# Kernel optimization log

Hardware: AMD Instinct MI355X
Metric: run time of the kernel (lower is better)

## Reference

```python
import jax, jax.numpy as jnp
import numpy as np

B, M_IN, H, W = 8, 63, 480, 640
VALID_FRAC = 0.05  # sparse-depth valid pixel density
N_ITERS = 5


def setup_inputs() -> dict:
    key = jax.random.key(0)
    k1, k2, k3 = jax.random.split(key, 3)
    bases = jax.random.normal(k1, (B, M_IN, H, W), dtype=jnp.float32)
    logit = jax.random.normal(k2, (B, 1, H, W), dtype=jnp.float32)
    valid = jax.random.uniform(k3, (B, 1, H, W)) < VALID_FRAC
    # invalid sparse-depth pixels -> log(0) = -inf, ignored via isfinite mask
    targets = jnp.where(valid, logit, -jnp.inf)
    return {"bases": bases, "targets": targets}


def _fit_single(basis, target):
    # basis: (m,h,w), target: (1,h,w)
    m = basis.shape[0]
    y = target[0]                                   # (h,w)
    mask = jnp.isfinite(y)
    maskf = mask.astype(basis.dtype)
    Xf = (basis * maskf).reshape(m, -1)             # masked basis, (m, hw)
    yf = jnp.where(mask, y, 0.0).reshape(-1)        # (hw,)
    XtX = Xf @ Xf.T                                 # (m,m) over valid pixels only
    Xty = Xf @ yf                                   # (m,)
    N = maskf.sum()

    # eval-mode EM-like refinement (prior.use == False): Tr_d = M / beta
    beta0 = jnp.sqrt(N)
    beta = beta0
    done = jnp.array(False)
    for _ in range(N_ITERS):
        w = jnp.linalg.solve(XtX * beta, Xty * beta)    # LU solve
        E_d = jnp.sum((yf - w @ Xf) ** 2)               # residual on valid pixels
        Tr_d = m / beta
        beta_new = N / (E_d + Tr_d)
        conv = jnp.abs(beta_new / beta0 - 1.0) < 0.02
        beta = jnp.where(done, beta, beta_new)
        beta0 = jnp.where(done, beta0, beta_new)
        done = done | conv

    A = XtX * beta
    w = jnp.linalg.solve(A, Xty * beta)                 # (m,)

    # recon3d: predicted log depth
    logit_pred = jnp.einsum('m,mhw->hw', w, basis)[None]  # (1,h,w)

    # pred_var: S_inv via Cholesky, var = (S_inv @ bt * bt).sum(0)
    L = jnp.linalg.cholesky(A)
    S_inv = jax.scipy.linalg.cho_solve((L, True), jnp.eye(m, dtype=basis.dtype))
    bt = basis.reshape(m, -1)                           # (m, hw)
    var = jnp.sum((S_inv @ bt) * bt, axis=0).reshape(1, basis.shape[1], basis.shape[2])
    return logit_pred, w, var


def reference(bases, targets):
    # th_homogenize(append=False): prepend a constant ones basis channel
    ones = jnp.ones_like(bases[:, :1])
    basis_h = jnp.concatenate([ones, bases], axis=1)    # (b, m+1, h, w)
    logits, weights, logit_var = jax.vmap(_fit_single)(basis_h, targets)
    return logits, weights, logit_var
```

## Files before the change

kernel.cpp:

```cpp
#include <hip/hip_runtime.h>
#include <cmath>

#define HW 307200
#define NB 8
#define NBASE 63
#define NCHUNK (HW/256)
#define GRAM_BLKS 128
#define QCAP 320

#define XTY_OFF 0
#define YTY_OFF (NB*64)
#define NC_OFF  (YTY_OFF + NB)
#define ZERO_FLOATS (NC_OFF + NB)
#define XTX_OFF ZERO_FLOATS
#define MP_OFF  (XTX_OFF + NB*64*64)
#define WV_OFF  (MP_OFF + NB*64*64)

#define OUT_W   (NB*HW)
#define OUT_VAR (OUT_W + NB*64)

__device__ __forceinline__ bool finitef(float x) {
    return (__float_as_uint(x) & 0x7f800000u) != 0x7f800000u;
}

__global__ __launch_bounds__(256) void gram_kernel(
    const float* __restrict__ bases, const float* __restrict__ targets,
    float* __restrict__ ws, float* __restrict__ part)
{
    __shared__ float tile[64*68];
    __shared__ float sy[64];
    __shared__ float qy[QCAP];
    __shared__ int   qidx[QCAP];
    __shared__ int   qn;

    const int t  = threadIdx.x;
    const int b  = blockIdx.y;
    const int wv = t >> 6;
    const int l  = t & 63;
    const int ti = l >> 3, tj = l & 7;

    float acc[8][8];
#pragma unroll
    for (int i = 0; i < 8; i++)
#pragma unroll
        for (int j = 0; j < 8; j++) acc[i][j] = 0.f;
    float acc_xty = 0.f, acc_yty = 0.f, acc_n = 0.f;

    const float* __restrict__ basesb = bases + (long)b * NBASE * HW;
    const float* __restrict__ targb  = targets + (long)b * HW;
    const long choff = (long)(l - 1) * HW;

    if (t == 0) qn = 0;
    __syncthreads();

    auto compute_tile = [&]() {
#pragma unroll 2
        for (int pp = 0; pp < 16; ++pp) {
            const int p2 = wv * 16 + pp;
            const float4 r0 = *(const float4*)&tile[p2*68 + 8*ti];
            const float4 r1 = *(const float4*)&tile[p2*68 + 8*ti + 4];
            const float4 c0 = *(const float4*)&tile[p2*68 + 8*tj];
            const float4 c1 = *(const float4*)&tile[p2*68 + 8*tj + 4];
            const float rr[8] = {r0.x,r0.y,r0.z,r0.w,r1.x,r1.y,r1.z,r1.w};
            const float cc[8] = {c0.x,c0.y,c0.z,c0.w,c1.x,c1.y,c1.z,c1.w};
#pragma unroll
            for (int i = 0; i < 8; i++)
#pragma unroll
                for (int j = 0; j < 8; j++)
                    acc[i][j] = fmaf(rr[i], cc[j], acc[i][j]);
            acc_xty = fmaf(sy[p2], tile[p2*68 + l], acc_xty);
        }
    };

    int qtot = 0;
    for (int j = blockIdx.x; j < NCHUNK; j += GRAM_BLKS) {
        const int p = j * 256 + t;
        const float y = targb[p];
        const bool fin = finitef(y);
        const unsigned long long m = __ballot(fin);
        int wbase = 0;
        if (l == 0) wbase = atomicAdd(&qn, __popcll(m));
        wbase = __shfl(wbase, 0, 64);
        if (fin) {
            const int r = __popcll(m & ((1ull << l) - 1ull));
            qidx[wbase + r] = p;
            qy[wbase + r]   = y;
            acc_yty = fmaf(y, y, acc_yty);
            acc_n += 1.f;
        }
        __syncthreads();
        qtot = qn;
        while (qtot >= 64) {
            const int base = qtot - 64;
            if (t < 64) sy[t] = qy[base + t];
#pragma unroll
            for (int pp = wv; pp < 64; pp += 4) {
                const int gp = qidx[base + pp];
                float v;
                if (l == 0) v = 1.f;
                else        v = basesb[choff + gp];
                tile[pp*68 + l] = v;
            }
            __syncthreads();
            compute_tile();
            qtot -= 64;
            __syncthreads();
        }
        if (t == 0) qn = qtot;
        __syncthreads();
    }

    if (qtot > 0) {
        if (t < 64) sy[t] = (t < qtot) ? qy[t] : 0.f;
#pragma unroll
        for (int pp = wv; pp < 64; pp += 4) {
            float v = 0.f;
            if (pp < qtot) {
                const int gp = qidx[pp];
                if (l == 0) v = 1.f;
                else        v = basesb[choff + gp];
            }
            tile[pp*68 + l] = v;
        }
        __syncthreads();
        compute_tile();
    }
    __syncthreads();

    for (int w = 0; w < 4; ++w) {
        if (wv == w) {
#pragma unroll
            for (int i = 0; i < 8; i++)
#pragma unroll
                for (int j2 = 0; j2 < 8; j2++) {
                    const int e = (8*ti + i) * 64 + 8*tj + j2;
                    tile[e] = (w == 0) ? acc[i][j2] : tile[e] + acc[i][j2];
                }
        }
        __syncthreads();
    }
    float* __restrict__ pb = part + (long)(b * GRAM_BLKS + blockIdx.x) * 4096;
#pragma unroll
    for (int k = 0; k < 4; ++k)
        *(float4*)&pb[t*16 + 4*k] = *(const float4*)&tile[t*16 + 4*k];

    for (int w = 0; w < 4; ++w) {
        if (wv == w) tile[4096 + l] = (w == 0) ? acc_xty : tile[4096 + l] + acc_xty;
        __syncthreads();
    }
    if (t < 64) atomicAdd(&ws[XTY_OFF + b*64 + t], tile[4096 + t]);

#pragma unroll
    for (int off = 32; off; off >>= 1) {
        acc_yty += __shfl_down(acc_yty, off, 64);
        acc_n   += __shfl_down(acc_n,   off, 64);
    }
    if (l == 0) {
        atomicAdd(&ws[YTY_OFF + b], acc_yty);
        atomicAdd(&ws[NC_OFF  + b], acc_n);
    }
}

__global__ __launch_bounds__(256) void reduce_kernel(
    const float* __restrict__ part, float* __restrict__ ws)
{
    const int b = blockIdx.y;
    const int e = blockIdx.x * 256 + threadIdx.x;
    const float* __restrict__ pb = part + (long)b * GRAM_BLKS * 4096 + e;
    float s = 0.f;
#pragma unroll 8
    for (int k = 0; k < GRAM_BLKS; ++k)
        s += pb[(long)k * 4096];
    ws[XTX_OFF + b*4096 + e] = s;
}

__global__ __launch_bounds__(64) void solve_kernel(
    float* __restrict__ ws, float* __restrict__ out)
{
    __shared__ float A[64*65];
    __shared__ float W[64*65];
    __shared__ float d0[64], xty[64], wv_s[64];

    const int b = blockIdx.x;
    const int t = threadIdx.x;
    const float* XtX = ws + XTX_OFF + b * 4096;

    for (int j = 0; j < 64; j++) A[t*65 + j] = XtX[t*64 + j];
    xty[t] = ws[XTY_OFF + b*64 + t];
    d0[t]  = A[t*65 + t];
    const float yty = ws[YTY_OFF + b];
    const float Nc  = ws[NC_OFF  + b];
    __syncthreads();

    for (int k = 0; k < 64; k++) {
        float akk = A[k*65 + k];
        __syncthreads();
        float dk = sqrtf(akk);
        if (t == k)      A[k*65 + k] = dk;
        else if (t > k)  A[t*65 + k] = A[t*65 + k] / dk;
        __syncthreads();
        if (t > k) {
            float ltk = A[t*65 + k];
            for (int j = k + 1; j <= t; j++)
                A[t*65 + j] -= ltk * A[j*65 + k];
        }
        __syncthreads();
    }

    for (int i = 0; i < 64; i++) {
        float s = (i == t) ? 1.f : 0.f;
        for (int j = 0; j < i; j++) s = fmaf(-A[i*65 + j], W[j*65 + t], s);
        W[i*65 + t] = s / A[i*65 + i];
    }
    for (int i = 63; i >= 0; i--) {
        float s = W[i*65 + t];
        for (int j = i + 1; j < 64; j++) s = fmaf(-A[j*65 + i], W[j*65 + t], s);
        W[i*65 + t] = s / A[i*65 + i];
    }
    __syncthreads();

    float wt = 0.f;
    for (int j = 0; j < 64; j++) wt = fmaf(W[t*65 + j], xty[j], wt);
    wv_s[t] = wt;
    __syncthreads();

    float qt = 0.f;
    for (int j = 0; j < 64; j++) {
        float x = (j > t) ? A[t*65 + j] : ((j == t) ? d0[t] : A[j*65 + t]);
        qt = fmaf(x, wv_s[j], qt);
    }
    float r1 = wt * xty[t];
    float r2 = wt * qt;
#pragma unroll
    for (int off = 32; off; off >>= 1) {
        r1 += __shfl_down(r1, off, 64);
        r2 += __shfl_down(r2, off, 64);
    }
    r1 = __shfl(r1, 0, 64);
    r2 = __shfl(r2, 0, 64);
    const float E_d = yty - 2.f * r1 + r2;

    float beta0 = sqrtf(Nc);
    float beta  = beta0;
    bool  done  = false;
#pragma unroll
    for (int it = 0; it < 5; ++it) {
        float Tr_d = 64.f / beta;
        float beta_new = Nc / (E_d + Tr_d);
        bool conv = fabsf(beta_new / beta0 - 1.f) < 0.02f;
        if (!done) { beta = beta_new; beta0 = beta_new; }
        done = done || conv;
    }
    const float ib = 1.f / beta;

    out[OUT_W + b*64 + t] = wt;
    ws[WV_OFF + b*64 + t] = wt;
    float* Mp = ws + MP_OFF + b * 4096;
    for (int j = 0; j < 64; j++) {
        float v = (j < t) ? 0.f : ((j == t) ? 0.5f : 1.f) * W[t*65 + j] * ib;
        Mp[t*64 + j] = v;
    }
}

__global__ __launch_bounds__(256) void predvar_kernel(
    const float* __restrict__ bases, const float* __restrict__ ws,
    float* __restrict__ out)
{
    const int b   = blockIdx.y;
    const int pix = blockIdx.x * 256 + threadIdx.x;
    const float* __restrict__ Mp = ws + MP_OFF + b * 4096;
    const float* __restrict__ wb = ws + WV_OFF + b * 64;
    const float* basesb = bases + (long)b * NBASE * HW + pix;

    float bv[64];
    bv[0] = 1.f;
#pragma unroll
    for (int c = 1; c < 64; c++) bv[c] = basesb[(long)(c - 1) * HW];

    float pred = wb[0];
#pragma unroll
    for (int c = 1; c < 64; c++) pred = fmaf(wb[c], bv[c], pred);

    float var2 = 0.f;
#pragma unroll
    for (int i = 0; i < 64; i++) {
        float si = 0.f;
#pragma unroll
        for (int j = i; j < 64; j++) si = fmaf(Mp[i*64 + j], bv[j], si);
        var2 = fmaf(si, bv[i], var2);
    }

    out[(long)b * HW + pix] = pred;
    out[OUT_VAR + (long)b * HW + pix] = 2.f * var2;
}

extern "C" void kernel_launch(void* const* d_in, const int* in_sizes, int n_in,
                              void* d_out, int out_size, void* d_ws, size_t ws_size,
                              hipStream_t stream)
{
    const float* bases   = (const float*)d_in[0];
    const float* targets = (const float*)d_in[1];
    float* out = (float*)d_out;
    float* ws  = (float*)d_ws;

    hipMemsetAsync(d_ws, 0, ZERO_FLOATS * sizeof(float), stream);

    gram_kernel<<<dim3(GRAM_BLKS, NB), 256, 0, stream>>>(bases, targets, ws, out);
    reduce_kernel<<<dim3(16, NB), 256, 0, stream>>>(out, ws);
    solve_kernel<<<NB, 64, 0, stream>>>(ws, out);
    predvar_kernel<<<dim3(HW / 256, NB), 256, 0, stream>>>(bases, ws, out);
}
```

Before: 579.1 us.

## Stage Mp in LDS, process two pixels per thread, widen Cholesky block

The pred-var kernel now copies the per-batch packed inverse matrix into shared memory and reads it as float4. Each thread handles two adjacent pixels with float2 loads, so every matrix element fetched is reused for two pixels. The solve kernel moves from 64 to 256 threads and splits the Cholesky trailing update and the final Mp write-out across four thread groups. The cost is a larger register footprint (two 64-float vectors per thread) under launch_bounds(256,2), which may cause spills or lower occupancy.

```diff
diff --git a/kernel.cpp b/kernel.cpp
--- a/kernel.cpp
+++ b/kernel.cpp
@@ -174,124 +174,158 @@
     ws[XTX_OFF + b*4096 + e] = s;
 }
 
-__global__ __launch_bounds__(64) void solve_kernel(
+__global__ __launch_bounds__(256) void solve_kernel(
     float* __restrict__ ws, float* __restrict__ out)
 {
     __shared__ float A[64*65];
     __shared__ float W[64*65];
-    __shared__ float d0[64], xty[64], wv_s[64];
+    __shared__ float d0[64], xty_s[64], wv_s[64];
+    __shared__ float ib_s;
 
     const int b = blockIdx.x;
     const int t = threadIdx.x;
+    const int r = t & 63;
+    const int q = t >> 6;
     const float* XtX = ws + XTX_OFF + b * 4096;
 
-    for (int j = 0; j < 64; j++) A[t*65 + j] = XtX[t*64 + j];
-    xty[t] = ws[XTY_OFF + b*64 + t];
-    d0[t]  = A[t*65 + t];
+    for (int e = t; e < 4096; e += 256)
+        A[(e >> 6) * 65 + (e & 63)] = XtX[e];
+    if (t < 64) xty_s[t] = ws[XTY_OFF + b*64 + t];
     const float yty = ws[YTY_OFF + b];
     const float Nc  = ws[NC_OFF  + b];
     __syncthreads();
+    if (t < 64) d0[t] = A[t*65 + t];
+    __syncthreads();
 
     for (int k = 0; k < 64; k++) {
-        float akk = A[k*65 + k];
-        __syncthreads();
-        float dk = sqrtf(akk);
-        if (t == k)      A[k*65 + k] = dk;
-        else if (t > k)  A[t*65 + k] = A[t*65 + k] / dk;
-        __syncthreads();
-        if (t > k) {
-            float ltk = A[t*65 + k];
-            for (int j = k + 1; j <= t; j++)
-                A[t*65 + j] -= ltk * A[j*65 + k];
-        }
-        __syncthreads();
-    }
-
-    for (int i = 0; i < 64; i++) {
-        float s = (i == t) ? 1.f : 0.f;
-        for (int j = 0; j < i; j++) s = fmaf(-A[i*65 + j], W[j*65 + t], s);
-        W[i*65 + t] = s / A[i*65 + i];
-    }
-    for (int i = 63; i >= 0; i--) {
-        float s = W[i*65 + t];
-        for (int j = i + 1; j < 64; j++) s = fmaf(-A[j*65 + i], W[j*65 + t], s);
-        W[i*65 + t] = s / A[i*65 + i];
-    }
-    __syncthreads();
-
-    float wt = 0.f;
-    for (int j = 0; j < 64; j++) wt = fmaf(W[t*65 + j], xty[j], wt);
-    wv_s[t] = wt;
-    __syncthreads();
-
-    float qt = 0.f;
-    for (int j = 0; j < 64; j++) {
-        float x = (j > t) ? A[t*65 + j] : ((j == t) ? d0[t] : A[j*65 + t]);
-        qt = fmaf(x, wv_s[j], qt);
-    }
-    float r1 = wt * xty[t];
-    float r2 = wt * qt;
-#pragma unroll
-    for (int off = 32; off; off >>= 1) {
-        r1 += __shfl_down(r1, off, 64);
-        r2 += __shfl_down(r2, off, 64);
-    }
-    r1 = __shfl(r1, 0, 64);
-    r2 = __shfl(r2, 0, 64);
-    const float E_d = yty - 2.f * r1 + r2;
-
-    float beta0 = sqrtf(Nc);
-    float beta  = beta0;
-    bool  done  = false;
-#pragma unroll
-    for (int it = 0; it < 5; ++it) {
-        float Tr_d = 64.f / beta;
-        float beta_new = Nc / (E_d + Tr_d);
-        bool conv = fabsf(beta_new / beta0 - 1.f) < 0.02f;
-        if (!done) { beta = beta_new; beta0 = beta_new; }
-        done = done || conv;
-    }
-    const float ib = 1.f / beta;
-
-    out[OUT_W + b*64 + t] = wt;
-    ws[WV_OFF + b*64 + t] = wt;
-    float* Mp = ws + MP_OFF + b * 4096;
-    for (int j = 0; j < 64; j++) {
-        float v = (j < t) ? 0.f : ((j == t) ? 0.5f : 1.f) * W[t*65 + j] * ib;
-        Mp[t*64 + j] = v;
-    }
-}
-
-__global__ __launch_bounds__(256) void predvar_kernel(
+        const float akk = A[k*65 + k];
+        __syncthreads();
+        const float dk = sqrtf(akk);
+        if (q == 0) {
+            if (r == k)     A[k*65 + k] = dk;
+            else if (r > k) A[r*65 + k] /= dk;
+        }
+        __syncthreads();
+        if (r > k) {
+            const float lrk = A[r*65 + k];
+            for (int j = k + 1 + q; j <= r; j += 4)
+                A[r*65 + j] -= lrk * A[j*65 + k];
+        }
+        __syncthreads();
+    }
+
+    if (q == 0) {
+        for (int i = 0; i < 64; i++) {
+            float s = (i == r) ? 1.f : 0.f;
+            for (int j = 0; j < i; j++) s = fmaf(-A[i*65 + j], W[j*65 + r], s);
+            W[i*65 + r] = s / A[i*65 + i];
+        }
+        for (int i = 63; i >= 0; i--) {
+            float s = W[i*65 + r];
+            for (int j = i + 1; j < 64; j++) s = fmaf(-A[j*65 + i], W[j*65 + r], s);
+            W[i*65 + r] = s / A[i*65 + i];
+        }
+        float wt = 0.f;
+        for (int j = 0; j < 64; j++) wt = fmaf(W[r*65 + j], xty_s[j], wt);
+        wv_s[r] = wt;
+
+        float qt = 0.f;
+        for (int j = 0; j < 64; j++) {
+            float x = (j > r) ? A[r*65 + j] : ((j == r) ? d0[r] : A[j*65 + r]);
+            qt = fmaf(x, wv_s[j], qt);
+        }
+        float r1 = wt * xty_s[r];
+        float r2 = wt * qt;
+#pragma unroll
+        for (int off = 32; off; off >>= 1) {
+            r1 += __shfl_down(r1, off, 64);
+            r2 += __shfl_down(r2, off, 64);
+        }
+        if (r == 0) {
+            const float E_d = yty - 2.f * r1 + r2;
+            float beta0 = sqrtf(Nc);
+            float beta  = beta0;
+            bool  done  = false;
+#pragma unroll
+            for (int it = 0; it < 5; ++it) {
+                float Tr_d = 64.f / beta;
+                float beta_new = Nc / (E_d + Tr_d);
+                bool conv = fabsf(beta_new / beta0 - 1.f) < 0.02f;
+                if (!done) { beta = beta_new; beta0 = beta_new; }
+                done = done || conv;
+            }
+            ib_s = 1.f / beta;
+        }
+        out[OUT_W + b*64 + r] = wt;
+        ws[WV_OFF + b*64 + r] = wt;
+    }
+    __syncthreads();
+
+    const float ib = ib_s;
+    float* __restrict__ Mp = ws + MP_OFF + b * 4096;
+    for (int e = t; e < 4096; e += 256) {
+        const int row = e >> 6, j = e & 63;
+        const float v = (j < row) ? 0.f
+                      : ((j == row) ? 0.5f : 1.f) * W[row*65 + j] * ib;
+        Mp[e] = v;
+    }
+}
+
+__global__ __launch_bounds__(256, 2) void predvar_kernel(
     const float* __restrict__ bases, const float* __restrict__ ws,
     float* __restrict__ out)
 {
-    const int b   = blockIdx.y;
-    const int pix = blockIdx.x * 256 + threadIdx.x;
-    const float* __restrict__ Mp = ws + MP_OFF + b * 4096;
-    const float* __restrict__ wb = ws + WV_OFF + b * 64;
+    __shared__ float Mp_s[4096];
+    __shared__ float w_s[64];
+
+    const int b = blockIdx.y;
+    const int t = threadIdx.x;
+    {
+        const float4* __restrict__ src = (const float4*)(ws + MP_OFF + b * 4096);
+        float4* dst = (float4*)Mp_s;
+        for (int e = t; e < 1024; e += 256) dst[e] = src[e];
+        if (t < 64) w_s[t] = ws[WV_OFF + b*64 + t];
+    }
+    __syncthreads();
+
+    const int pix = (blockIdx.x * 256 + t) * 2;
     const float* basesb = bases + (long)b * NBASE * HW + pix;
 
-    float bv[64];
-    bv[0] = 1.f;
-#pragma unroll
-    for (int c = 1; c < 64; c++) bv[c] = basesb[(long)(c - 1) * HW];
-
-    float pred = wb[0];
-#pragma unroll
-    for (int c = 1; c < 64; c++) pred = fmaf(wb[c], bv[c], pred);
-
-    float var2 = 0.f;
+    float2 bv[64];
+    bv[0] = make_float2(1.f, 1.f);
+#pragma unroll
+    for (int c = 1; c < 64; c++)
+        bv[c] = *(const float2*)&basesb[(long)(c - 1) * HW];
+
+    float px = w_s[0], py = w_s[0];
+#pragma unroll
+    for (int c = 1; c < 64; c++) {
+        px = fmaf(w_s[c], bv[c].x, px);
+        py = fmaf(w_s[c], bv[c].y, py);
+    }
+
+    float vx = 0.f, vy = 0.f;
 #pragma unroll
     for (int i = 0; i < 64; i++) {
-        float si = 0.f;
-#pragma unroll
-        for (int j = i; j < 64; j++) si = fmaf(Mp[i*64 + j], bv[j], si);
-        var2 = fmaf(si, bv[i], var2);
-    }
-
-    out[(long)b * HW + pix] = pred;
-    out[OUT_VAR + (long)b * HW + pix] = 2.f * var2;
+        float sx = 0.f, sy2 = 0.f;
+#pragma unroll
+        for (int qd = i >> 2; qd < 16; qd++) {
+            const float4 m = *(const float4*)&Mp_s[i*64 + 4*qd];
+            sx  = fmaf(m.x, bv[4*qd+0].x, sx);
+            sy2 = fmaf(m.x, bv[4*qd+0].y, sy2);
+            sx  = fmaf(m.y, bv[4*qd+1].x, sx);
+            sy2 = fmaf(m.y, bv[4*qd+1].y, sy2);
+            sx  = fmaf(m.z, bv[4*qd+2].x, sx);
+            sy2 = fmaf(m.z, bv[4*qd+2].y, sy2);
+            sx  = fmaf(m.w, bv[4*qd+3].x, sx);
+            sy2 = fmaf(m.w, bv[4*qd+3].y, sy2);
+        }
+        vx = fmaf(sx,  bv[i].x, vx);
+        vy = fmaf(sy2, bv[i].y, vy);
+    }
+
+    *(float2*)&out[(long)b * HW + pix] = make_float2(px, py);
+    *(float2*)&out[OUT_VAR + (long)b * HW + pix] = make_float2(2.f * vx, 2.f * vy);
 }
 
 extern "C" void kernel_launch(void* const* d_in, const int* in_sizes, int n_in,
@@ -307,6 +341,6 @@
 
     gram_kernel<<<dim3(GRAM_BLKS, NB), 256, 0, stream>>>(bases, targets, ws, out);
     reduce_kernel<<<dim3(16, NB), 256, 0, stream>>>(out, ws);
-    solve_kernel<<<NB, 64, 0, stream>>>(ws, out);
-    predvar_kernel<<<dim3(HW / 256, NB), 256, 0, stream>>>(bases, ws, out);
-}
+    solve_kernel<<<NB, 256, 0, stream>>>(ws, out);
+    predvar_kernel<<<dim3(HW / 512, NB), 256, 0, stream>>>(bases, ws, out);
+}
```

After: 578.3 us. Within noise of the previous version (-0.1%).

## Register-block predvar over 4 pixels with LDS-staged matrix; register-based triangular inverse

Applied to the files above, without the earlier changes.

The pred/var kernel now processes four pixels per thread with float4 loads and stores, and stages the per-batch quadratic-form matrix in shared memory so each matrix element is reused across four pixels. The solve kernel keeps each thread's inverse column in registers, with unrolled multi-accumulator loops and reciprocal diagonals, and writes the matrix transposed for coalesced stores. The aim is to cut instruction and memory overhead in the dominant per-pixel quadratic form. The risk is very high register pressure from 64 float4 values per thread, which may spill or reduce occupancy.

```diff
diff --git a/kernel.cpp b/kernel.cpp
--- a/kernel.cpp
+++ b/kernel.cpp
@@ -178,58 +178,95 @@
     float* __restrict__ ws, float* __restrict__ out)
 {
     __shared__ float A[64*65];
-    __shared__ float W[64*65];
-    __shared__ float d0[64], xty[64], wv_s[64];
+    __shared__ float d0[64], dinv_s[64], xty_s[64], wv_s[64];
 
     const int b = blockIdx.x;
     const int t = threadIdx.x;
     const float* XtX = ws + XTX_OFF + b * 4096;
 
-    for (int j = 0; j < 64; j++) A[t*65 + j] = XtX[t*64 + j];
-    xty[t] = ws[XTY_OFF + b*64 + t];
-    d0[t]  = A[t*65 + t];
+    for (int e = t; e < 4096; e += 64)
+        A[(e >> 6) * 65 + (e & 63)] = XtX[e];
+    xty_s[t] = ws[XTY_OFF + b*64 + t];
     const float yty = ws[YTY_OFF + b];
     const float Nc  = ws[NC_OFF  + b];
     __syncthreads();
+    d0[t] = A[t*65 + t];
+    __syncthreads();
 
     for (int k = 0; k < 64; k++) {
-        float akk = A[k*65 + k];
-        __syncthreads();
-        float dk = sqrtf(akk);
+        const float akk = A[k*65 + k];
+        __syncthreads();
+        const float dk = sqrtf(akk);
         if (t == k)      A[k*65 + k] = dk;
-        else if (t > k)  A[t*65 + k] = A[t*65 + k] / dk;
+        else if (t > k)  A[t*65 + k] /= dk;
         __syncthreads();
         if (t > k) {
-            float ltk = A[t*65 + k];
+            const float ltk = A[t*65 + k];
             for (int j = k + 1; j <= t; j++)
                 A[t*65 + j] -= ltk * A[j*65 + k];
         }
         __syncthreads();
     }
 
+    dinv_s[t] = 1.f / A[t*65 + t];
+    __syncthreads();
+
+    float Wc[64];
+#pragma unroll
     for (int i = 0; i < 64; i++) {
-        float s = (i == t) ? 1.f : 0.f;
-        for (int j = 0; j < i; j++) s = fmaf(-A[i*65 + j], W[j*65 + t], s);
-        W[i*65 + t] = s / A[i*65 + i];
-    }
+        float s0 = (i == t) ? 1.f : 0.f, s1 = 0.f, s2 = 0.f, s3 = 0.f;
+        const int nfull = i >> 2;
+#pragma unroll
+        for (int qd = 0; qd < nfull; qd++) {
+            const int j = qd * 4;
+            s0 = fmaf(-A[i*65 + j    ], Wc[j    ], s0);
+            s1 = fmaf(-A[i*65 + j + 1], Wc[j + 1], s1);
+            s2 = fmaf(-A[i*65 + j + 2], Wc[j + 2], s2);
+            s3 = fmaf(-A[i*65 + j + 3], Wc[j + 3], s3);
+        }
+#pragma unroll
+        for (int j = nfull * 4; j < i; j++)
+            s0 = fmaf(-A[i*65 + j], Wc[j], s0);
+        Wc[i] = ((s0 + s1) + (s2 + s3)) * dinv_s[i];
+    }
+#pragma unroll
     for (int i = 63; i >= 0; i--) {
-        float s = W[i*65 + t];
-        for (int j = i + 1; j < 64; j++) s = fmaf(-A[j*65 + i], W[j*65 + t], s);
-        W[i*65 + t] = s / A[i*65 + i];
-    }
-    __syncthreads();
-
-    float wt = 0.f;
-    for (int j = 0; j < 64; j++) wt = fmaf(W[t*65 + j], xty[j], wt);
+        float s0 = Wc[i], s1 = 0.f, s2 = 0.f, s3 = 0.f;
+        const int j0 = i + 1;
+        const int nfull = (64 - j0) >> 2;
+#pragma unroll
+        for (int qd = 0; qd < nfull; qd++) {
+            const int j = j0 + qd * 4;
+            s0 = fmaf(-A[(j    )*65 + i], Wc[j    ], s0);
+            s1 = fmaf(-A[(j + 1)*65 + i], Wc[j + 1], s1);
+            s2 = fmaf(-A[(j + 2)*65 + i], Wc[j + 2], s2);
+            s3 = fmaf(-A[(j + 3)*65 + i], Wc[j + 3], s3);
+        }
+#pragma unroll
+        for (int j = j0 + nfull * 4; j < 64; j++)
+            s0 = fmaf(-A[j*65 + i], Wc[j], s0);
+        Wc[i] = ((s0 + s1) + (s2 + s3)) * dinv_s[i];
+    }
+
+    float w0 = 0.f, w1 = 0.f, w2 = 0.f, w3 = 0.f;
+#pragma unroll
+    for (int j = 0; j < 64; j += 4) {
+        w0 = fmaf(Wc[j    ], xty_s[j    ], w0);
+        w1 = fmaf(Wc[j + 1], xty_s[j + 1], w1);
+        w2 = fmaf(Wc[j + 2], xty_s[j + 2], w2);
+        w3 = fmaf(Wc[j + 3], xty_s[j + 3], w3);
+    }
+    const float wt = (w0 + w1) + (w2 + w3);
     wv_s[t] = wt;
     __syncthreads();
 
     float qt = 0.f;
+#pragma unroll
     for (int j = 0; j < 64; j++) {
-        float x = (j > t) ? A[t*65 + j] : ((j == t) ? d0[t] : A[j*65 + t]);
+        const float x = (j > t) ? A[t*65 + j] : ((j == t) ? d0[t] : A[j*65 + t]);
         qt = fmaf(x, wv_s[j], qt);
     }
-    float r1 = wt * xty[t];
+    float r1 = wt * xty_s[t];
     float r2 = wt * qt;
 #pragma unroll
     for (int off = 32; off; off >>= 1) {
@@ -245,9 +282,9 @@
     bool  done  = false;
 #pragma unroll
     for (int it = 0; it < 5; ++it) {
-        float Tr_d = 64.f / beta;
-        float beta_new = Nc / (E_d + Tr_d);
-        bool conv = fabsf(beta_new / beta0 - 1.f) < 0.02f;
+        const float Tr_d = 64.f / beta;
+        const float beta_new = Nc / (E_d + Tr_d);
+        const bool conv = fabsf(beta_new / beta0 - 1.f) < 0.02f;
         if (!done) { beta = beta_new; beta0 = beta_new; }
         done = done || conv;
     }
@@ -255,10 +292,11 @@
 
     out[OUT_W + b*64 + t] = wt;
     ws[WV_OFF + b*64 + t] = wt;
-    float* Mp = ws + MP_OFF + b * 4096;
+    float* __restrict__ Mp = ws + MP_OFF + b * 4096;
+#pragma unroll
     for (int j = 0; j < 64; j++) {
-        float v = (j < t) ? 0.f : ((j == t) ? 0.5f : 1.f) * W[t*65 + j] * ib;
-        Mp[t*64 + j] = v;
+        const float v = (j > t) ? 0.f : ((j == t) ? 0.5f : 1.f) * Wc[j] * ib;
+        Mp[j*64 + t] = v;
     }
 }
 
@@ -266,32 +304,70 @@
     const float* __restrict__ bases, const float* __restrict__ ws,
     float* __restrict__ out)
 {
-    const int b   = blockIdx.y;
-    const int pix = blockIdx.x * 256 + threadIdx.x;
-    const float* __restrict__ Mp = ws + MP_OFF + b * 4096;
-    const float* __restrict__ wb = ws + WV_OFF + b * 64;
+    __shared__ float Mp_s[4096];
+    __shared__ float w_s[64];
+
+    const int b = blockIdx.y;
+    const int t = threadIdx.x;
+    {
+        const float4* __restrict__ src = (const float4*)(ws + MP_OFF + b * 4096);
+        float4* dst = (float4*)Mp_s;
+        for (int e = t; e < 1024; e += 256) dst[e] = src[e];
+        if (t < 64) w_s[t] = ws[WV_OFF + b*64 + t];
+    }
+    __syncthreads();
+
+    const int pix = (blockIdx.x * 256 + t) * 4;
     const float* basesb = bases + (long)b * NBASE * HW + pix;
 
-    float bv[64];
-    bv[0] = 1.f;
-#pragma unroll
-    for (int c = 1; c < 64; c++) bv[c] = basesb[(long)(c - 1) * HW];
-
-    float pred = wb[0];
-#pragma unroll
-    for (int c = 1; c < 64; c++) pred = fmaf(wb[c], bv[c], pred);
-
-    float var2 = 0.f;
+    float4 bv[64];
+    bv[0] = make_float4(1.f, 1.f, 1.f, 1.f);
+#pragma unroll
+    for (int c = 1; c < 64; c++)
+        bv[c] = *(const float4*)&basesb[(long)(c - 1) * HW];
+
+    float4 pr = make_float4(w_s[0], w_s[0], w_s[0], w_s[0]);
+#pragma unroll
+    for (int c = 1; c < 64; c++) {
+        pr.x = fmaf(w_s[c], bv[c].x, pr.x);
+        pr.y = fmaf(w_s[c], bv[c].y, pr.y);
+        pr.z = fmaf(w_s[c], bv[c].z, pr.z);
+        pr.w = fmaf(w_s[c], bv[c].w, pr.w);
+    }
+
+    float4 vr = make_float4(0.f, 0.f, 0.f, 0.f);
 #pragma unroll
     for (int i = 0; i < 64; i++) {
-        float si = 0.f;
-#pragma unroll
-        for (int j = i; j < 64; j++) si = fmaf(Mp[i*64 + j], bv[j], si);
-        var2 = fmaf(si, bv[i], var2);
-    }
-
-    out[(long)b * HW + pix] = pred;
-    out[OUT_VAR + (long)b * HW + pix] = 2.f * var2;
+        float4 s = make_float4(0.f, 0.f, 0.f, 0.f);
+#pragma unroll
+        for (int qd = i >> 2; qd < 16; qd++) {
+            const float4 m = *(const float4*)&Mp_s[i*64 + 4*qd];
+            s.x = fmaf(m.x, bv[4*qd+0].x, s.x);
+            s.y = fmaf(m.x, bv[4*qd+0].y, s.y);
+            s.z = fmaf(m.x, bv[4*qd+0].z, s.z);
+            s.w = fmaf(m.x, bv[4*qd+0].w, s.w);
+            s.x = fmaf(m.y, bv[4*qd+1].x, s.x);
+            s.y = fmaf(m.y, bv[4*qd+1].y, s.y);
+            s.z = fmaf(m.y, bv[4*qd+1].z, s.z);
+            s.w = fmaf(m.y, bv[4*qd+1].w, s.w);
+            s.x = fmaf(m.z, bv[4*qd+2].x, s.x);
+            s.y = fmaf(m.z, bv[4*qd+2].y, s.y);
+            s.z = fmaf(m.z, bv[4*qd+2].z, s.z);
+            s.w = fmaf(m.z, bv[4*qd+2].w, s.w);
+            s.x = fmaf(m.w, bv[4*qd+3].x, s.x);
+            s.y = fmaf(m.w, bv[4*qd+3].y, s.y);
+            s.z = fmaf(m.w, bv[4*qd+3].z, s.z);
+            s.w = fmaf(m.w, bv[4*qd+3].w, s.w);
+        }
+        vr.x = fmaf(s.x, bv[i].x, vr.x);
+        vr.y = fmaf(s.y, bv[i].y, vr.y);
+        vr.z = fmaf(s.z, bv[i].z, vr.z);
+        vr.w = fmaf(s.w, bv[i].w, vr.w);
+    }
+
+    *(float4*)&out[(long)b * HW + pix] = pr;
+    *(float4*)&out[OUT_VAR + (long)b * HW + pix] =
+        make_float4(2.f * vr.x, 2.f * vr.y, 2.f * vr.z, 2.f * vr.w);
 }
 
 extern "C" void kernel_launch(void* const* d_in, const int* in_sizes, int n_in,
@@ -308,5 +384,5 @@
     gram_kernel<<<dim3(GRAM_BLKS, NB), 256, 0, stream>>>(bases, targets, ws, out);
     reduce_kernel<<<dim3(16, NB), 256, 0, stream>>>(out, ws);
     solve_kernel<<<NB, 64, 0, stream>>>(ws, out);
-    predvar_kernel<<<dim3(HW / 256, NB), 256, 0, stream>>>(bases, ws, out);
-}
+    predvar_kernel<<<dim3(HW / 1024, NB), 256, 0, stream>>>(bases, ws, out);
+}
```

Measured after the change: 665.5 us. +14.9%, slower.
